# Performance work log

Hardware: AMD Instinct MI355X
Metric: run time of the kernel (lower is better)

## Reference

```python
import jax, jax.numpy as jnp
import numpy as np

HEAD_DIM = 64
R = 4            # region_token_num
THETA = 10000.0


def _rope_cos_sin(pos, D, theta):
    # pos: [B, L] int -> cos/sin [B, 1, L, D] (half-split / GPT-NeoX layout)
    inv_freq = theta ** (-(jnp.arange(0, D, 2, dtype=jnp.float32) / D))  # [D/2]
    ang = pos.astype(jnp.float32)[..., None] * inv_freq                  # [B, L, D/2]
    cos = jnp.concatenate([jnp.cos(ang), jnp.cos(ang)], axis=-1)[:, None]
    sin = jnp.concatenate([jnp.sin(ang), jnp.sin(ang)], axis=-1)[:, None]
    return cos, sin


def _apply_rope(x, cos, sin):
    # x: [B, H, L, D]
    D = x.shape[-1]
    x1, x2 = x[..., : D // 2], x[..., D // 2 :]
    rot = jnp.concatenate([-x2, x1], axis=-1)
    return x * cos + rot * sin


def _local_positions(regions):
    # index within contiguous region run: [B, T]
    B, T = regions.shape
    idx = jnp.arange(T, dtype=jnp.int32)
    is_new = jnp.concatenate(
        [jnp.ones((B, 1), bool), regions[:, 1:] != regions[:, :-1]], axis=1
    )
    start = jax.lax.cummax(jnp.where(is_new, idx[None, :], 0), axis=1)
    return idx[None, :] - start


def reference(query_q, x_k, x_v, regions, t_mask, n_mask, max_n):
    B, H, P, D = query_q.shape
    T = regions.shape[1]

    # ---- local RoPE positions: pool tokens all 0 (use_pool_offset=False),
    # x tokens: local index within region + R, zeroed on pads
    pool_pos = jnp.zeros((B, P), dtype=jnp.int32)
    x_pos = (_local_positions(regions) + R) * (regions > 0).astype(jnp.int32)

    cq, sq = _rope_cos_sin(pool_pos, D, THETA)
    ck, sk = _rope_cos_sin(x_pos, D, THETA)
    q = _apply_rope(query_q, cq, sq)
    k = _apply_rope(x_k, ck, sk)

    # ---- block-diagonal (same-region) cross-attention mask [B, 1, P, T]
    pool_region = jnp.repeat(jnp.arange(1, max_n + 1, dtype=regions.dtype), R)  # [P]
    pool_valid = jnp.repeat(n_mask, R, axis=1)                                   # [B, P]
    same = pool_region[None, :, None] == regions[:, None, :]
    valid = pool_valid[:, :, None] & t_mask[:, None, :]
    non_pad = (pool_region != 0)[None, :, None] & (regions != 0)[:, None, :]
    mask = (same & valid & non_pad)[:, None]                                     # [B,1,P,T]

    # ---- SDPA
    scale = 1.0 / jnp.sqrt(jnp.asarray(D, jnp.float32))
    scores = jnp.einsum('bhpd,bhtd->bhpt', q, k) * scale
    scores = jnp.where(mask, scores, jnp.asarray(-1e30, scores.dtype))
    attn = jax.nn.softmax(scores, axis=-1)
    return jnp.einsum('bhpt,bhtd->bhpd', attn, x_v)


def setup_inputs() -> dict:
    key = jax.random.key(0)
    k1, k2, k3, k4 = jax.random.split(key, 4)
    B, H, T, max_n = 4, 16, 4096, 64
    P = max_n * R
    regions = jnp.sort(jax.random.randint(k4, (B, T), 0, 65), axis=1)
    return {
        'query_q': jax.random.normal(k1, (B, H, P, HEAD_DIM), jnp.float32),
        'x_k': jax.random.normal(k2, (B, H, T, HEAD_DIM), jnp.float32),
        'x_v': jax.random.normal(k3, (B, H, T, HEAD_DIM), jnp.float32),
        'regions': regions,
        't_mask': jnp.ones((B, T), dtype=bool),
        'n_mask': jnp.ones((B, max_n), dtype=bool),
        'max_n': max_n,
    }
```

## Files before the change

### kernel.cpp

```cpp
#include <hip/hip_runtime.h>
#include <math.h>

#define NB   4
#define NH   16
#define NT   4096
#define ND   64
#define NP   256
#define NREG 64
#define RPOS 4

#define INVF_LOG2 0.4152410118609203f
#define QSCALE 0.18033688011112042f

__global__ void seg_kernel(const int* __restrict__ regions, int* __restrict__ bound) {
    const int b = blockIdx.x;
    const int* rb = regions + b * NT;
    int* bb = bound + b * 66;
    if (threadIdx.x < 66) bb[threadIdx.x] = NT;
    __syncthreads();
    for (int i = threadIdx.x; i < NT; i += blockDim.x) {
        const int r  = rb[i];
        const int rp = (i == 0) ? -1 : rb[i - 1];
        for (int v = rp + 1; v <= r; ++v) bb[v] = i;
    }
}

__global__ __launch_bounds__(256, 4) void lca_kernel(
    const float* __restrict__ q,
    const float* __restrict__ k,
    const float* __restrict__ v,
    const int*   __restrict__ bound,
    float*       __restrict__ out)
{
    const int tid  = threadIdx.x;
    const int wave = tid >> 6;
    const int lane = tid & 63;
    const int grp  = lane >> 3;
    const int li   = lane & 7;
    const int dlo  = li << 2;

    const int blk = blockIdx.x;
    const int rg  = blk & 15;
    const int h   = (blk >> 4) & (NH - 1);
    const int b   = blk >> 8;
    const int ri  = (rg << 2) + wave;
    const int p0  = ri << 2;

    const int s   = bound[b * 66 + ri + 1];
    const int e   = bound[b * 66 + ri + 2];
    const int cnt = e - s;

    const size_t bh = (size_t)(b * NH + h);
    const float* kb = k + bh * (size_t)(NT * ND);
    const float* vb = v + bh * (size_t)(NT * ND);
    const float* qb = q + (bh * NP + p0) * ND;

    float l[4] = {0.f, 0.f, 0.f, 0.f};
    float acc[4][8];
    #pragma unroll
    for (int p = 0; p < 4; ++p)
        #pragma unroll
        for (int i = 0; i < 8; ++i) acc[p][i] = 0.f;

    if (cnt > 0) {
        float qs[4][8];
        #pragma unroll
        for (int p = 0; p < 4; ++p) {
            const float4 qa = *(const float4*)(qb + p * ND + dlo);
            const float4 qc = *(const float4*)(qb + p * ND + 32 + dlo);
            qs[p][0] = qa.x * QSCALE; qs[p][1] = qa.y * QSCALE;
            qs[p][2] = qa.z * QSCALE; qs[p][3] = qa.w * QSCALE;
            qs[p][4] = qc.x * QSCALE; qs[p][5] = qc.y * QSCALE;
            qs[p][6] = qc.z * QSCALE; qs[p][7] = qc.w * QSCALE;
        }
        float frq[4];
        #pragma unroll
        for (int i = 0; i < 4; ++i)
            frq[i] = exp2f(-INVF_LOG2 * (float)(dlo + i));

        const int iters = (cnt + 7) >> 3;

        int t0c = min(s + grp, e - 1);
        const float* kp = kb + (size_t)t0c * ND;
        const float* vp = vb + (size_t)t0c * ND;
        float4 ka = *(const float4*)(kp + dlo);
        float4 kc = *(const float4*)(kp + 32 + dlo);
        float4 va = *(const float4*)(vp + dlo);
        float4 vc = *(const float4*)(vp + 32 + dlo);

        for (int it = 0; it < iters; ++it) {
            const int tn = min(s + ((it + 1) << 3) + grp, e - 1);
            const float* nkp = kb + (size_t)tn * ND;
            const float* nvp = vb + (size_t)tn * ND;
            const float4 nka = *(const float4*)(nkp + dlo);
            const float4 nkc = *(const float4*)(nkp + 32 + dlo);
            const float4 nva = *(const float4*)(nvp + dlo);
            const float4 nvc = *(const float4*)(nvp + 32 + dlo);

            const int   t     = s + (it << 3) + grp;
            const bool  valid = t < e;
            const float pos   = (float)(min(t, e - 1) - s + RPOS);

            const float klo[4] = {ka.x, ka.y, ka.z, ka.w};
            const float khi[4] = {kc.x, kc.y, kc.z, kc.w};
            float pd0 = 0.f, pd1 = 0.f, pd2 = 0.f, pd3 = 0.f;
            #pragma unroll
            for (int i = 0; i < 4; ++i) {
                float sa, ca;
                __sincosf(pos * frq[i], &sa, &ca);
                const float rlo = klo[i] * ca - khi[i] * sa;
                const float rhi = khi[i] * ca + klo[i] * sa;
                pd0 = fmaf(rlo, qs[0][i], fmaf(rhi, qs[0][i + 4], pd0));
                pd1 = fmaf(rlo, qs[1][i], fmaf(rhi, qs[1][i + 4], pd1));
                pd2 = fmaf(rlo, qs[2][i], fmaf(rhi, qs[2][i + 4], pd2));
                pd3 = fmaf(rlo, qs[3][i], fmaf(rhi, qs[3][i + 4], pd3));
            }
            #pragma unroll
            for (int m = 1; m <= 4; m <<= 1) {
                pd0 += __shfl_xor(pd0, m);
                pd1 += __shfl_xor(pd1, m);
                pd2 += __shfl_xor(pd2, m);
                pd3 += __shfl_xor(pd3, m);
            }
            const float w0 = valid ? exp2f(pd0) : 0.f;
            const float w1 = valid ? exp2f(pd1) : 0.f;
            const float w2 = valid ? exp2f(pd2) : 0.f;
            const float w3 = valid ? exp2f(pd3) : 0.f;
            l[0] += w0; l[1] += w1; l[2] += w2; l[3] += w3;
            const float vx[8] = {va.x, va.y, va.z, va.w, vc.x, vc.y, vc.z, vc.w};
            #pragma unroll
            for (int i = 0; i < 8; ++i) {
                acc[0][i] = fmaf(w0, vx[i], acc[0][i]);
                acc[1][i] = fmaf(w1, vx[i], acc[1][i]);
                acc[2][i] = fmaf(w2, vx[i], acc[2][i]);
                acc[3][i] = fmaf(w3, vx[i], acc[3][i]);
            }
            ka = nka; kc = nkc; va = nva; vc = nvc;
        }
    } else {
        for (int t = grp; t < NT; t += 8) {
            const float* vp = vb + (size_t)t * ND;
            const float4 va = *(const float4*)(vp + dlo);
            const float4 vc = *(const float4*)(vp + 32 + dlo);
            acc[0][0] += va.x; acc[0][1] += va.y; acc[0][2] += va.z; acc[0][3] += va.w;
            acc[0][4] += vc.x; acc[0][5] += vc.y; acc[0][6] += vc.z; acc[0][7] += vc.w;
        }
        #pragma unroll
        for (int p = 1; p < 4; ++p)
            #pragma unroll
            for (int i = 0; i < 8; ++i) acc[p][i] = acc[0][i];
        l[0] = l[1] = l[2] = l[3] = (float)NT * 0.125f;
    }

    #pragma unroll
    for (int m = 8; m <= 32; m <<= 1) {
        #pragma unroll
        for (int p = 0; p < 4; ++p) {
            l[p] += __shfl_xor(l[p], m);
            #pragma unroll
            for (int i = 0; i < 8; ++i) acc[p][i] += __shfl_xor(acc[p][i], m);
        }
    }

    #pragma unroll
    for (int p = 0; p < 4; ++p) {
        if (grp == p) {
            const float inv = 1.f / l[p];
            float* op = out + (bh * NP + p0 + p) * ND;
            *(float4*)(op + dlo) = make_float4(acc[p][0] * inv, acc[p][1] * inv,
                                               acc[p][2] * inv, acc[p][3] * inv);
            *(float4*)(op + 32 + dlo) = make_float4(acc[p][4] * inv, acc[p][5] * inv,
                                                    acc[p][6] * inv, acc[p][7] * inv);
        }
    }
}

extern "C" void kernel_launch(void* const* d_in, const int* in_sizes, int n_in,
                              void* d_out, int out_size, void* d_ws, size_t ws_size,
                              hipStream_t stream) {
    (void)in_sizes; (void)n_in; (void)ws_size; (void)out_size;
    const float* q       = (const float*)d_in[0];
    const float* k       = (const float*)d_in[1];
    const float* v       = (const float*)d_in[2];
    const int*   regions = (const int*)d_in[3];
    float* out   = (float*)d_out;
    int*   bound = (int*)d_ws;

    seg_kernel<<<dim3(NB), 1024, 0, stream>>>(regions, bound);
    lca_kernel<<<dim3(NB * NH * (NREG / 4)), 256, 0, stream>>>(q, k, v, bound, out);
}
```

Baseline: 35.12 us.

## Split each region's tokens across two waves and combine partials in shared memory

Each region is now processed by two waves instead of one. Each wave handles half of the region's token range, and the partial accumulators and denominators are merged through shared memory before the output is written. The grid doubles to 2048 blocks, which raises parallelism and shortens the serial per-wave loop, so long regions should stop dominating latency. In exchange it adds a __syncthreads, shared-memory traffic and a duplicated Q load per region. The launch_bounds occupancy hint is also dropped.

```diff
diff --git a/kernel.cpp b/kernel.cpp
--- a/kernel.cpp
+++ b/kernel.cpp
@@ -25,13 +25,16 @@
     }
 }
 
-__global__ __launch_bounds__(256, 4) void lca_kernel(
+__global__ __launch_bounds__(256) void lca_kernel(
     const float* __restrict__ q,
     const float* __restrict__ k,
     const float* __restrict__ v,
     const int*   __restrict__ bound,
     float*       __restrict__ out)
 {
+    __shared__ float pacc[4][4][64];
+    __shared__ float pl[4][4];
+
     const int tid  = threadIdx.x;
     const int wave = tid >> 6;
     const int lane = tid & 63;
@@ -40,22 +43,34 @@
     const int dlo  = li << 2;
 
     const int blk = blockIdx.x;
-    const int rg  = blk & 15;
-    const int h   = (blk >> 4) & (NH - 1);
-    const int b   = blk >> 8;
-    const int ri  = (rg << 2) + wave;
+    const int rgp = blk & 31;
+    const int h   = (blk >> 5) & (NH - 1);
+    const int b   = blk >> 9;
+    const int ri  = (rgp << 1) + (wave >> 1);
+    const int w   = wave & 1;
     const int p0  = ri << 2;
-
-    const int s   = bound[b * 66 + ri + 1];
-    const int e   = bound[b * 66 + ri + 2];
-    const int cnt = e - s;
 
     const size_t bh = (size_t)(b * NH + h);
     const float* kb = k + bh * (size_t)(NT * ND);
     const float* vb = v + bh * (size_t)(NT * ND);
     const float* qb = q + (bh * NP + p0) * ND;
 
-    float l[4] = {0.f, 0.f, 0.f, 0.f};
+    float qs[4][8];
+    #pragma unroll
+    for (int p = 0; p < 4; ++p) {
+        const float4 qa = *(const float4*)(qb + p * ND + dlo);
+        const float4 qc = *(const float4*)(qb + p * ND + 32 + dlo);
+        qs[p][0] = qa.x * QSCALE; qs[p][1] = qa.y * QSCALE;
+        qs[p][2] = qa.z * QSCALE; qs[p][3] = qa.w * QSCALE;
+        qs[p][4] = qc.x * QSCALE; qs[p][5] = qc.y * QSCALE;
+        qs[p][6] = qc.z * QSCALE; qs[p][7] = qc.w * QSCALE;
+    }
+
+    const int s   = bound[b * 66 + ri + 1];
+    const int e   = bound[b * 66 + ri + 2];
+    const int cnt = e - s;
+
+    float l4[4] = {0.f, 0.f, 0.f, 0.f};
     float acc[4][8];
     #pragma unroll
     for (int p = 0; p < 4; ++p)
@@ -63,82 +78,78 @@
         for (int i = 0; i < 8; ++i) acc[p][i] = 0.f;
 
     if (cnt > 0) {
-        float qs[4][8];
-        #pragma unroll
-        for (int p = 0; p < 4; ++p) {
-            const float4 qa = *(const float4*)(qb + p * ND + dlo);
-            const float4 qc = *(const float4*)(qb + p * ND + 32 + dlo);
-            qs[p][0] = qa.x * QSCALE; qs[p][1] = qa.y * QSCALE;
-            qs[p][2] = qa.z * QSCALE; qs[p][3] = qa.w * QSCALE;
-            qs[p][4] = qc.x * QSCALE; qs[p][5] = qc.y * QSCALE;
-            qs[p][6] = qc.z * QSCALE; qs[p][7] = qc.w * QSCALE;
-        }
-        float frq[4];
-        #pragma unroll
-        for (int i = 0; i < 4; ++i)
-            frq[i] = exp2f(-INVF_LOG2 * (float)(dlo + i));
-
-        const int iters = (cnt + 7) >> 3;
-
-        int t0c = min(s + grp, e - 1);
-        const float* kp = kb + (size_t)t0c * ND;
-        const float* vp = vb + (size_t)t0c * ND;
-        float4 ka = *(const float4*)(kp + dlo);
-        float4 kc = *(const float4*)(kp + 32 + dlo);
-        float4 va = *(const float4*)(vp + dlo);
-        float4 vc = *(const float4*)(vp + 32 + dlo);
-
-        for (int it = 0; it < iters; ++it) {
-            const int tn = min(s + ((it + 1) << 3) + grp, e - 1);
-            const float* nkp = kb + (size_t)tn * ND;
-            const float* nvp = vb + (size_t)tn * ND;
-            const float4 nka = *(const float4*)(nkp + dlo);
-            const float4 nkc = *(const float4*)(nkp + 32 + dlo);
-            const float4 nva = *(const float4*)(nvp + dlo);
-            const float4 nvc = *(const float4*)(nvp + 32 + dlo);
-
-            const int   t     = s + (it << 3) + grp;
-            const bool  valid = t < e;
-            const float pos   = (float)(min(t, e - 1) - s + RPOS);
-
-            const float klo[4] = {ka.x, ka.y, ka.z, ka.w};
-            const float khi[4] = {kc.x, kc.y, kc.z, kc.w};
-            float pd0 = 0.f, pd1 = 0.f, pd2 = 0.f, pd3 = 0.f;
-            #pragma unroll
-            for (int i = 0; i < 4; ++i) {
-                float sa, ca;
-                __sincosf(pos * frq[i], &sa, &ca);
-                const float rlo = klo[i] * ca - khi[i] * sa;
-                const float rhi = khi[i] * ca + klo[i] * sa;
-                pd0 = fmaf(rlo, qs[0][i], fmaf(rhi, qs[0][i + 4], pd0));
-                pd1 = fmaf(rlo, qs[1][i], fmaf(rhi, qs[1][i + 4], pd1));
-                pd2 = fmaf(rlo, qs[2][i], fmaf(rhi, qs[2][i + 4], pd2));
-                pd3 = fmaf(rlo, qs[3][i], fmaf(rhi, qs[3][i + 4], pd3));
+        const int hlen  = ((cnt + 15) >> 4) << 3;
+        const int ms    = s + w * hlen;
+        const int me    = min(e, ms + hlen);
+        const int mycnt = me - ms;
+        if (mycnt > 0) {
+            float frq[4];
+            #pragma unroll
+            for (int i = 0; i < 4; ++i)
+                frq[i] = exp2f(-INVF_LOG2 * (float)(dlo + i));
+
+            const int iters = (mycnt + 7) >> 3;
+
+            const int t0c = min(ms + grp, e - 1);
+            const float* kp = kb + (size_t)t0c * ND;
+            const float* vp = vb + (size_t)t0c * ND;
+            float4 ka = *(const float4*)(kp + dlo);
+            float4 kc = *(const float4*)(kp + 32 + dlo);
+            float4 va = *(const float4*)(vp + dlo);
+            float4 vc = *(const float4*)(vp + 32 + dlo);
+
+            for (int it = 0; it < iters; ++it) {
+                const int tn = min(ms + ((it + 1) << 3) + grp, e - 1);
+                const float* nkp = kb + (size_t)tn * ND;
+                const float* nvp = vb + (size_t)tn * ND;
+                const float4 nka = *(const float4*)(nkp + dlo);
+                const float4 nkc = *(const float4*)(nkp + 32 + dlo);
+                const float4 nva = *(const float4*)(nvp + dlo);
+                const float4 nvc = *(const float4*)(nvp + 32 + dlo);
+
+                const int   t     = ms + (it << 3) + grp;
+                const bool  valid = t < me;
+                const float pos   = (float)(min(t, e - 1) - s + RPOS);
+
+                const float klo[4] = {ka.x, ka.y, ka.z, ka.w};
+                const float khi[4] = {kc.x, kc.y, kc.z, kc.w};
+                float pd0 = 0.f, pd1 = 0.f, pd2 = 0.f, pd3 = 0.f;
+                #pragma unroll
+                for (int i = 0; i < 4; ++i) {
+                    float sa, ca;
+                    __sincosf(pos * frq[i], &sa, &ca);
+                    const float rlo = klo[i] * ca - khi[i] * sa;
+                    const float rhi = khi[i] * ca + klo[i] * sa;
+                    pd0 = fmaf(rlo, qs[0][i], fmaf(rhi, qs[0][i + 4], pd0));
+                    pd1 = fmaf(rlo, qs[1][i], fmaf(rhi, qs[1][i + 4], pd1));
+                    pd2 = fmaf(rlo, qs[2][i], fmaf(rhi, qs[2][i + 4], pd2));
+                    pd3 = fmaf(rlo, qs[3][i], fmaf(rhi, qs[3][i + 4], pd3));
+                }
+                #pragma unroll
+                for (int m = 1; m <= 4; m <<= 1) {
+                    pd0 += __shfl_xor(pd0, m);
+                    pd1 += __shfl_xor(pd1, m);
+                    pd2 += __shfl_xor(pd2, m);
+                    pd3 += __shfl_xor(pd3, m);
+                }
+                const float w0 = valid ? exp2f(pd0) : 0.f;
+                const float w1 = valid ? exp2f(pd1) : 0.f;
+                const float w2 = valid ? exp2f(pd2) : 0.f;
+                const float w3 = valid ? exp2f(pd3) : 0.f;
+                l4[0] += w0; l4[1] += w1; l4[2] += w2; l4[3] += w3;
+                const float vx[8] = {va.x, va.y, va.z, va.w, vc.x, vc.y, vc.z, vc.w};
+                #pragma unroll
+                for (int i = 0; i < 8; ++i) {
+                    acc[0][i] = fmaf(w0, vx[i], acc[0][i]);
+                    acc[1][i] = fmaf(w1, vx[i], acc[1][i]);
+                    acc[2][i] = fmaf(w2, vx[i], acc[2][i]);
+                    acc[3][i] = fmaf(w3, vx[i], acc[3][i]);
+                }
+                ka = nka; kc = nkc; va = nva; vc = nvc;
             }
-            #pragma unroll
-            for (int m = 1; m <= 4; m <<= 1) {
-                pd0 += __shfl_xor(pd0, m);
-                pd1 += __shfl_xor(pd1, m);
-                pd2 += __shfl_xor(pd2, m);
-                pd3 += __shfl_xor(pd3, m);
-            }
-            const float w0 = valid ? exp2f(pd0) : 0.f;
-            const float w1 = valid ? exp2f(pd1) : 0.f;
-            const float w2 = valid ? exp2f(pd2) : 0.f;
-            const float w3 = valid ? exp2f(pd3) : 0.f;
-            l[0] += w0; l[1] += w1; l[2] += w2; l[3] += w3;
-            const float vx[8] = {va.x, va.y, va.z, va.w, vc.x, vc.y, vc.z, vc.w};
-            #pragma unroll
-            for (int i = 0; i < 8; ++i) {
-                acc[0][i] = fmaf(w0, vx[i], acc[0][i]);
-                acc[1][i] = fmaf(w1, vx[i], acc[1][i]);
-                acc[2][i] = fmaf(w2, vx[i], acc[2][i]);
-                acc[3][i] = fmaf(w3, vx[i], acc[3][i]);
-            }
-            ka = nka; kc = nkc; va = nva; vc = nvc;
         }
     } else {
-        for (int t = grp; t < NT; t += 8) {
+        for (int t = (w << 3) + grp; t < NT; t += 16) {
             const float* vp = vb + (size_t)t * ND;
             const float4 va = *(const float4*)(vp + dlo);
             const float4 vc = *(const float4*)(vp + 32 + dlo);
@@ -149,29 +160,47 @@
         for (int p = 1; p < 4; ++p)
             #pragma unroll
             for (int i = 0; i < 8; ++i) acc[p][i] = acc[0][i];
-        l[0] = l[1] = l[2] = l[3] = (float)NT * 0.125f;
+        l4[0] = l4[1] = l4[2] = l4[3] = (float)NT / 16.f;
     }
 
     #pragma unroll
     for (int m = 8; m <= 32; m <<= 1) {
         #pragma unroll
         for (int p = 0; p < 4; ++p) {
-            l[p] += __shfl_xor(l[p], m);
+            l4[p] += __shfl_xor(l4[p], m);
             #pragma unroll
             for (int i = 0; i < 8; ++i) acc[p][i] += __shfl_xor(acc[p][i], m);
         }
     }
 
-    #pragma unroll
-    for (int p = 0; p < 4; ++p) {
-        if (grp == p) {
-            const float inv = 1.f / l[p];
-            float* op = out + (bh * NP + p0 + p) * ND;
-            *(float4*)(op + dlo) = make_float4(acc[p][0] * inv, acc[p][1] * inv,
-                                               acc[p][2] * inv, acc[p][3] * inv);
-            *(float4*)(op + 32 + dlo) = make_float4(acc[p][4] * inv, acc[p][5] * inv,
-                                                    acc[p][6] * inv, acc[p][7] * inv);
-        }
+    if (grp == 0) {
+        #pragma unroll
+        for (int p = 0; p < 4; ++p) {
+            *(float4*)&pacc[wave][p][dlo] =
+                make_float4(acc[p][0], acc[p][1], acc[p][2], acc[p][3]);
+            *(float4*)&pacc[wave][p][32 + dlo] =
+                make_float4(acc[p][4], acc[p][5], acc[p][6], acc[p][7]);
+        }
+        if (li == 0) {
+            #pragma unroll
+            for (int p = 0; p < 4; ++p) pl[wave][p] = l4[p];
+        }
+    }
+    __syncthreads();
+
+    if (tid < 128) {
+        const int rg2  = tid >> 6;
+        const int pool = (tid >> 4) & 3;
+        const int d    = (tid & 15) << 2;
+        const int wA   = rg2 << 1, wB = wA + 1;
+        const float lsum = pl[wA][pool] + pl[wB][pool];
+        const float inv  = 1.f / lsum;
+        const float4 a = *(const float4*)&pacc[wA][pool][d];
+        const float4 c = *(const float4*)&pacc[wB][pool][d];
+        const int   po = ((rgp << 1) + rg2) * 4 + pool;
+        *(float4*)(out + (bh * NP + po) * ND + d) =
+            make_float4((a.x + c.x) * inv, (a.y + c.y) * inv,
+                        (a.z + c.z) * inv, (a.w + c.w) * inv);
     }
 }
 
@@ -187,5 +216,5 @@
     int*   bound = (int*)d_ws;
 
     seg_kernel<<<dim3(NB), 1024, 0, stream>>>(regions, bound);
-    lca_kernel<<<dim3(NB * NH * (NREG / 4)), 256, 0, stream>>>(q, k, v, bound, out);
+    lca_kernel<<<dim3(NB * NH * (NREG / 2)), 256, 0, stream>>>(q, k, v, bound, out);
 }
```

New measurement: 36.29 us. 1.03x slower.

## Split each region's four queries across two waves to double parallelism

Applied to the files above, without the earlier changes.

Each wave now handles two pool queries of a region instead of four, so two waves share one region and the grid doubles. Register use per thread falls, and the launch bound rises to 8 blocks per CU for more occupancy. The cost is that each region's K/V is loaded twice, and the RoPE sincos work is duplicated across the wave pair. The q load is also hoisted ahead of the bound lookup.

```diff
diff --git a/kernel.cpp b/kernel.cpp
--- a/kernel.cpp
+++ b/kernel.cpp
@@ -25,7 +25,7 @@
     }
 }
 
-__global__ __launch_bounds__(256, 4) void lca_kernel(
+__global__ __launch_bounds__(256, 8) void lca_kernel(
     const float* __restrict__ q,
     const float* __restrict__ k,
     const float* __restrict__ v,
@@ -40,39 +40,41 @@
     const int dlo  = li << 2;
 
     const int blk = blockIdx.x;
-    const int rg  = blk & 15;
-    const int h   = (blk >> 4) & (NH - 1);
-    const int b   = blk >> 8;
-    const int ri  = (rg << 2) + wave;
-    const int p0  = ri << 2;
-
-    const int s   = bound[b * 66 + ri + 1];
-    const int e   = bound[b * 66 + ri + 2];
-    const int cnt = e - s;
+    const int rgp = blk & 31;
+    const int h   = (blk >> 5) & (NH - 1);
+    const int b   = blk >> 9;
+    const int ri  = (rgp << 1) + (wave >> 1);
+    const int ph  = wave & 1;
+    const int p0  = (ri << 2) + (ph << 1);
 
     const size_t bh = (size_t)(b * NH + h);
     const float* kb = k + bh * (size_t)(NT * ND);
     const float* vb = v + bh * (size_t)(NT * ND);
     const float* qb = q + (bh * NP + p0) * ND;
 
-    float l[4] = {0.f, 0.f, 0.f, 0.f};
-    float acc[4][8];
+    float qs[2][8];
     #pragma unroll
-    for (int p = 0; p < 4; ++p)
+    for (int p = 0; p < 2; ++p) {
+        const float4 qa = *(const float4*)(qb + p * ND + dlo);
+        const float4 qc = *(const float4*)(qb + p * ND + 32 + dlo);
+        qs[p][0] = qa.x * QSCALE; qs[p][1] = qa.y * QSCALE;
+        qs[p][2] = qa.z * QSCALE; qs[p][3] = qa.w * QSCALE;
+        qs[p][4] = qc.x * QSCALE; qs[p][5] = qc.y * QSCALE;
+        qs[p][6] = qc.z * QSCALE; qs[p][7] = qc.w * QSCALE;
+    }
+
+    const int s   = bound[b * 66 + ri + 1];
+    const int e   = bound[b * 66 + ri + 2];
+    const int cnt = e - s;
+
+    float l4[2] = {0.f, 0.f};
+    float acc[2][8];
+    #pragma unroll
+    for (int p = 0; p < 2; ++p)
         #pragma unroll
         for (int i = 0; i < 8; ++i) acc[p][i] = 0.f;
 
     if (cnt > 0) {
-        float qs[4][8];
-        #pragma unroll
-        for (int p = 0; p < 4; ++p) {
-            const float4 qa = *(const float4*)(qb + p * ND + dlo);
-            const float4 qc = *(const float4*)(qb + p * ND + 32 + dlo);
-            qs[p][0] = qa.x * QSCALE; qs[p][1] = qa.y * QSCALE;
-            qs[p][2] = qa.z * QSCALE; qs[p][3] = qa.w * QSCALE;
-            qs[p][4] = qc.x * QSCALE; qs[p][5] = qc.y * QSCALE;
-            qs[p][6] = qc.z * QSCALE; qs[p][7] = qc.w * QSCALE;
-        }
         float frq[4];
         #pragma unroll
         for (int i = 0; i < 4; ++i)
@@ -80,7 +82,7 @@
 
         const int iters = (cnt + 7) >> 3;
 
-        int t0c = min(s + grp, e - 1);
+        const int t0c = min(s + grp, e - 1);
         const float* kp = kb + (size_t)t0c * ND;
         const float* vp = vb + (size_t)t0c * ND;
         float4 ka = *(const float4*)(kp + dlo);
@@ -103,7 +105,7 @@
 
             const float klo[4] = {ka.x, ka.y, ka.z, ka.w};
             const float khi[4] = {kc.x, kc.y, kc.z, kc.w};
-            float pd0 = 0.f, pd1 = 0.f, pd2 = 0.f, pd3 = 0.f;
+            float pd0 = 0.f, pd1 = 0.f;
             #pragma unroll
             for (int i = 0; i < 4; ++i) {
                 float sa, ca;
@@ -112,28 +114,20 @@
                 const float rhi = khi[i] * ca + klo[i] * sa;
                 pd0 = fmaf(rlo, qs[0][i], fmaf(rhi, qs[0][i + 4], pd0));
                 pd1 = fmaf(rlo, qs[1][i], fmaf(rhi, qs[1][i + 4], pd1));
-                pd2 = fmaf(rlo, qs[2][i], fmaf(rhi, qs[2][i + 4], pd2));
-                pd3 = fmaf(rlo, qs[3][i], fmaf(rhi, qs[3][i + 4], pd3));
             }
             #pragma unroll
             for (int m = 1; m <= 4; m <<= 1) {
                 pd0 += __shfl_xor(pd0, m);
                 pd1 += __shfl_xor(pd1, m);
-                pd2 += __shfl_xor(pd2, m);
-                pd3 += __shfl_xor(pd3, m);
             }
             const float w0 = valid ? exp2f(pd0) : 0.f;
             const float w1 = valid ? exp2f(pd1) : 0.f;
-            const float w2 = valid ? exp2f(pd2) : 0.f;
-            const float w3 = valid ? exp2f(pd3) : 0.f;
-            l[0] += w0; l[1] += w1; l[2] += w2; l[3] += w3;
+            l4[0] += w0; l4[1] += w1;
             const float vx[8] = {va.x, va.y, va.z, va.w, vc.x, vc.y, vc.z, vc.w};
             #pragma unroll
             for (int i = 0; i < 8; ++i) {
                 acc[0][i] = fmaf(w0, vx[i], acc[0][i]);
                 acc[1][i] = fmaf(w1, vx[i], acc[1][i]);
-                acc[2][i] = fmaf(w2, vx[i], acc[2][i]);
-                acc[3][i] = fmaf(w3, vx[i], acc[3][i]);
             }
             ka = nka; kc = nkc; va = nva; vc = nvc;
         }
@@ -146,26 +140,24 @@
             acc[0][4] += vc.x; acc[0][5] += vc.y; acc[0][6] += vc.z; acc[0][7] += vc.w;
         }
         #pragma unroll
-        for (int p = 1; p < 4; ++p)
-            #pragma unroll
-            for (int i = 0; i < 8; ++i) acc[p][i] = acc[0][i];
-        l[0] = l[1] = l[2] = l[3] = (float)NT * 0.125f;
+        for (int i = 0; i < 8; ++i) acc[1][i] = acc[0][i];
+        l4[0] = l4[1] = (float)NT * 0.125f;
     }
 
     #pragma unroll
     for (int m = 8; m <= 32; m <<= 1) {
         #pragma unroll
-        for (int p = 0; p < 4; ++p) {
-            l[p] += __shfl_xor(l[p], m);
+        for (int p = 0; p < 2; ++p) {
+            l4[p] += __shfl_xor(l4[p], m);
             #pragma unroll
             for (int i = 0; i < 8; ++i) acc[p][i] += __shfl_xor(acc[p][i], m);
         }
     }
 
-    #pragma unroll
-    for (int p = 0; p < 4; ++p) {
-        if (grp == p) {
-            const float inv = 1.f / l[p];
+    if (grp == 0) {
+        #pragma unroll
+        for (int p = 0; p < 2; ++p) {
+            const float inv = 1.f / l4[p];
             float* op = out + (bh * NP + p0 + p) * ND;
             *(float4*)(op + dlo) = make_float4(acc[p][0] * inv, acc[p][1] * inv,
                                                acc[p][2] * inv, acc[p][3] * inv);
@@ -187,5 +179,5 @@
     int*   bound = (int*)d_ws;
 
     seg_kernel<<<dim3(NB), 1024, 0, stream>>>(regions, bound);
-    lca_kernel<<<dim3(NB * NH * (NREG / 4)), 256, 0, stream>>>(q, k, v, bound, out);
+    lca_kernel<<<dim3(NB * NH * (NREG / 2)), 256, 0, stream>>>(q, k, v, bound, out);
 }
```

New measurement: 49.82 us. +41.8%, slower.
